# Kernel tuning notes

Hardware: AMD Instinct MI355X
Metric: run time of the kernel (lower is better)

## Reference

```python
import jax, jax.numpy as jnp
import numpy as np

B, S, HID = 2, 2048, 2048
NH, NKV, HD = 16, 16, 128
SCALE = 1.0 / np.sqrt(HD)


def _rotate_half(x):
    x1, x2 = jnp.split(x, 2, axis=-1)
    return jnp.concatenate([-x2, x1], axis=-1)


def setup_inputs() -> dict:
    key = jax.random.key(0)
    k1, k2, k3 = jax.random.split(key, 3)
    hidden_states = jax.random.normal(k1, (B, S, HID), dtype=jnp.float32)
    # standard RoPE cos/sin tables, shape [S, HD]
    inv_freq = 1.0 / (10000.0 ** (np.arange(0, HD, 2, dtype=np.float32) / HD))
    freqs = np.outer(np.arange(S, dtype=np.float32), inv_freq)  # [S, HD/2]
    emb = np.concatenate([freqs, freqs], axis=-1)               # [S, HD]
    cos = jnp.asarray(np.cos(emb), dtype=jnp.float32)
    sin = jnp.asarray(np.sin(emb), dtype=jnp.float32)
    # torch Linear weights are [out, in]; forward computes x @ W.T
    w_qkv = jax.random.normal(k2, ((NH + 2 * NKV) * HD, HID), dtype=jnp.float32) * 0.02
    w_o = jax.random.normal(k3, (HID, NH * HD), dtype=jnp.float32) * 0.02
    return {"hidden_states": hidden_states, "cos": cos, "sin": sin,
            "w_qkv": w_qkv, "w_o": w_o}


def reference(hidden_states, cos, sin, w_qkv, w_o):
    b, s, _ = hidden_states.shape
    qkv = hidden_states @ w_qkv.T                         # [B,S,(NH+2*NKV)*HD]
    qkv = qkv.reshape(b, s, NH + 2 * NKV, HD)
    q = qkv[:, :, :NH]                                    # [B,S,NH,HD]
    k = qkv[:, :, NH:NH + NKV]                            # [B,S,NKV,HD]
    v = qkv[:, :, NH + NKV:]                              # [B,S,NKV,HD]
    # RoPE: broadcast cos/sin [S,HD] -> [1,S,1,HD]
    c = cos[None, :, None, :]
    sn = sin[None, :, None, :]
    q = q * c + _rotate_half(q) * sn
    k = k * c + _rotate_half(k) * sn
    scores = jnp.einsum("bihd,bjhd->bhij", q, k) * SCALE  # [B,H,S,S]
    attn = jax.nn.softmax(scores, axis=-1)
    out = jnp.einsum("bhij,bjhd->bihd", attn, v)          # [B,S,H,HD]
    out = out.reshape(b, s, NH * HD)
    return out @ w_o.T                                    # [B,S,HID]
```

## Files before the change

kernel.cpp:

```cpp
#include <hip/hip_runtime.h>
#include <hip/hip_bf16.h>

typedef float f32x4 __attribute__((ext_vector_type(4)));
typedef __bf16 bf16x8 __attribute__((ext_vector_type(8)));
typedef __bf16 bf16x4 __attribute__((ext_vector_type(4)));

#define S_LEN 2048
#define NHEADS 16
#define HDIM 128
#define KLOG2E (0.08838834764831845f * 1.4426950408889634f)
#define MSHIFT 2.0f

__device__ __forceinline__ void gld_lds16(const __bf16* g, __bf16* l) {
  __builtin_amdgcn_global_load_lds(
      (__attribute__((address_space(1))) void*)(void*)g,
      (__attribute__((address_space(3))) void*)l,
      16, 0, 0);
}

template <int N>
__device__ __forceinline__ void waitv() {
  if constexpr (N == 8)      asm volatile("s_waitcnt vmcnt(8)" ::: "memory");
  else if constexpr (N == 6) asm volatile("s_waitcnt vmcnt(6)" ::: "memory");
  else if constexpr (N == 4) asm volatile("s_waitcnt vmcnt(4)" ::: "memory");
  else if constexpr (N == 3) asm volatile("s_waitcnt vmcnt(3)" ::: "memory");
  else                       asm volatile("s_waitcnt vmcnt(0)" ::: "memory");
}

__global__ __launch_bounds__(256)
void cvt_all(const float* __restrict__ i0, __bf16* __restrict__ o0,
             const float* __restrict__ i1, __bf16* __restrict__ o1,
             const float* __restrict__ i2, __bf16* __restrict__ o2) {
  int i = (blockIdx.x * 256 + threadIdx.x) * 4;
  if (i >= 25165824) return;
  const float* in;
  __bf16* out;
  if (i < 8388608)       { in = i0 + i;              out = o0 + i; }
  else if (i < 20971520) { in = i1 + (i - 8388608);  out = o1 + (i - 8388608); }
  else                   { in = i2 + (i - 20971520); out = o2 + (i - 20971520); }
  float4 v = *(const float4*)in;
  bf16x4 o;
  o[0] = (__bf16)v.x; o[1] = (__bf16)v.y; o[2] = (__bf16)v.z; o[3] = (__bf16)v.w;
  *(bf16x4*)out = o;
}

template <int MREP, bool RMAP>
__device__ __forceinline__ void gemm_core(const __bf16* __restrict__ A,
                                          const __bf16* __restrict__ B,
                                          __bf16* lds, int am0, int bn0,
                                          f32x4 (&acc)[MREP][4]) {
  constexpr int K = 2048;
  constexpr int AF = MREP * 2;
  constexpr int SLOT = (AF + 16) * 512;
  constexpr int NA = AF / 8;
  constexpr int NL = NA + 2;
  const int tid = threadIdx.x;
  const int w = tid >> 6, lane = tid & 63;
  const int l15 = lane & 15;
  const int wm = w >> 2, wn = w & 3;

  const __bf16* asrc = A + (size_t)(am0 + l15) * K + (lane >> 4) * 8;
  const __bf16* bsrc = B + (size_t)(bn0 + l15) * K + (lane >> 4) * 8;

  auto stage = [&](int t) {
    __bf16* s = lds + (t & 3) * SLOT;
#pragma unroll
    for (int i = 0; i < NA; ++i) {
      const int f = w * NA + i;
      gld_lds16(asrc + (size_t)f * (16 * K) + t * 32, s + f * 512 + lane * 8);
    }
#pragma unroll
    for (int i = 0; i < 2; ++i) {
      const int g = w * 2 + i;
      gld_lds16(bsrc + (size_t)g * (16 * K) + t * 32, s + (AF + g) * 512 + lane * 8);
    }
  };

  stage(0); stage(1); stage(2);
  waitv<2 * NL>();
  __builtin_amdgcn_s_barrier();

  for (int t = 0; t < 64; ++t) {
    if (t < 61) stage(t + 3);
    const __bf16* s = lds + (t & 3) * SLOT + lane * 8;
    const __bf16* sB = s + AF * 512;
    bf16x8 bfr[4];
#pragma unroll
    for (int j = 0; j < 4; ++j) {
      const int g = RMAP ? ((wn >> 1) * 8 + (wn & 1) * 2 + (j & 1) + (j >> 1) * 4)
                         : (wn * 4 + j);
      bfr[j] = *(const bf16x8*)(sB + g * 512);
    }
#pragma unroll
    for (int half = 0; half < MREP / 4; ++half) {
      bf16x8 af[4];
#pragma unroll
      for (int i = 0; i < 4; ++i)
        af[i] = *(const bf16x8*)(s + (wm * MREP + half * 4 + i) * 512);
      __builtin_amdgcn_s_setprio(1);
#pragma unroll
      for (int i = 0; i < 4; ++i)
#pragma unroll
        for (int j = 0; j < 4; ++j)
          acc[half * 4 + i][j] = __builtin_amdgcn_mfma_f32_16x16x32_bf16(
              af[i], bfr[j], acc[half * 4 + i][j], 0, 0, 0);
      __builtin_amdgcn_s_setprio(0);
    }
    if (t < 63) {
      if (t < 61)       waitv<2 * NL>();
      else if (t == 61) waitv<NL>();
      else              waitv<0>();
      __builtin_amdgcn_s_barrier();
    }
  }
}


__global__ __launch_bounds__(512)
void gemm_bt_qkp(const __bf16* __restrict__ A, const __bf16* __restrict__ B,
                 __bf16* __restrict__ Qp, __bf16* __restrict__ Kp,
                 const float* __restrict__ cosp, const float* __restrict__ sinp) {
  __shared__ alignas(16) char smem[139264];
  const int am0 = blockIdx.y * 256;
  const int bn0 = blockIdx.x * 256;
  const int tid = threadIdx.x;
  const int w = tid >> 6, lane = tid & 63;
  const int l15 = lane & 15, quad = lane >> 4;
  const int wm = w >> 2, wn = w & 3;
  f32x4 acc[8][4] = {};
  gemm_core<8, true>(A, B, (__bf16*)smem, am0, bn0, acc);

  __syncthreads();
  float* csb = (float*)smem;
  float* snb = csb + 256 * 68;
  const int sbase = am0 & 2047;
  for (int q = tid; q < 4096; q += 512) {
    const int row = q >> 4, dq = (q & 15) * 4;
    *(float4*)(csb + row * 68 + dq) =
        *(const float4*)(cosp + (size_t)(sbase + row) * 128 + dq);
    *(float4*)(snb + row * 68 + dq) =
        *(const float4*)(sinp + (size_t)(sbase + row) * 128 + dq);
  }
  __syncthreads();

  const int head_sel = wn >> 1;
  const int hcol0 = bn0 + head_sel * 128;
  const int head = hcol0 >> 7;
  const int h = head & 15;
  __bf16* dst = (head < 16) ? Qp : Kp;
#pragma unroll
  for (int i = 0; i < 8; ++i) {
    const int row_b = am0 + wm * 128 + i * 16 + quad * 4;
    const int bidx = row_b >> 11;
    const int s = row_b & 2047;
    const int sl = wm * 128 + i * 16 + quad * 4;
    const int s16 = s >> 4;
    const int l15p0 = s & 15;
#pragma unroll
    for (int j2 = 0; j2 < 2; ++j2) {
      const int dl = (wn & 1) * 32 + j2 * 16 + l15;
      const int dh = dl + 64;
      const int kkl = dl >> 5, qpl = (dl >> 3) & 3, el = dl & 7;
      const int kkh = dh >> 5, qph = (dh >> 3) & 3, eh = dh & 7;
      const size_t base_lo =
          (((size_t)((bidx * 16 + h) * 128 + s16) * 4 + kkl) * 64 + qpl * 16 + l15p0) * 8 + el;
      const size_t base_hi =
          (((size_t)((bidx * 16 + h) * 128 + s16) * 4 + kkh) * 64 + qph * 16 + l15p0) * 8 + eh;
#pragma unroll
      for (int r = 0; r < 4; ++r) {
        const float c = csb[(sl + r) * 68 + dl];
        const float sn = snb[(sl + r) * 68 + dl];
        const float a = acc[i][j2][r], bb = acc[i][j2 + 2][r];
        dst[base_lo + (size_t)r * 8] = (__bf16)(a * c - bb * sn);
        dst[base_hi + (size_t)r * 8] = (__bf16)(bb * c + a * sn);
      }
    }
  }
}

__global__ __launch_bounds__(512)
void gemm_bt_vp(const __bf16* __restrict__ A, const __bf16* __restrict__ B,
                __bf16* __restrict__ Vp) {
  __shared__ alignas(16) __bf16 lds[4 * 24 * 512];
  const int am0 = blockIdx.y * 128;
  const int bn0 = blockIdx.x * 256;
  const int tid = threadIdx.x;
  const int w = tid >> 6, lane = tid & 63;
  const int l15 = lane & 15, quad = lane >> 4;
  const int wm = w >> 2, wn = w & 3;
  f32x4 acc[4][4] = {};
  gemm_core<4, false>(A, B, lds, am0, bn0, acc);
#pragma unroll
  for (int i = 0; i < 4; ++i) {
    const int row_b = am0 + wm * 64 + i * 16 + quad * 4;
    const int b = row_b >> 11;
    const int key0 = row_b & 2047;
    const int quadp = (key0 >> 3) & 3;
    const int kkv = key0 >> 5;
    const int e0 = key0 & 7;
#pragma unroll
    for (int j = 0; j < 4; ++j) {
      const int col = bn0 + wn * 64 + j * 16 + l15;
      const int h = col >> 7, dd = col & 127;
      const int tt = dd >> 4, l15p = dd & 15;
      bf16x4 o;
#pragma unroll
      for (int r = 0; r < 4; ++r) o[r] = (__bf16)acc[i][j][r];
      size_t addr = (((size_t)((b * 16 + h) * 8 + tt) * 64 + kkv) * 64
                     + quadp * 16 + l15p) * 8 + e0;
      *(bf16x4*)(Vp + addr) = o;
    }
  }
}

__global__ __launch_bounds__(512)
void gemm_bt_f(const __bf16* __restrict__ A, const __bf16* __restrict__ B,
               float* __restrict__ C) {
  __shared__ alignas(16) __bf16 lds[4 * 24 * 512];
  const int am0 = blockIdx.y * 128;
  const int bn0 = blockIdx.x * 256;
  const int tid = threadIdx.x;
  const int w = tid >> 6, lane = tid & 63;
  const int l15 = lane & 15, quad = lane >> 4;
  const int wm = w >> 2, wn = w & 3;
  f32x4 acc[4][4] = {};
  gemm_core<4, false>(A, B, lds, am0, bn0, acc);
#pragma unroll
  for (int i = 0; i < 4; ++i) {
    const int row_b = am0 + wm * 64 + i * 16 + quad * 4;
#pragma unroll
    for (int j = 0; j < 4; ++j) {
      const int col = bn0 + wn * 64 + j * 16 + l15;
#pragma unroll
      for (int r = 0; r < 4; ++r)
        C[(size_t)(row_b + r) * 2048 + col] = acc[i][j][r];
    }
  }
}

__global__ __launch_bounds__(512)
void attn_kernel(const __bf16* __restrict__ Qp, const __bf16* __restrict__ Kp,
                 const __bf16* __restrict__ Vp, __bf16* __restrict__ O) {
  const int lid = blockIdx.x;
  const int qt = (lid >> 3) & 7;
  const int bh = (lid & 7) * 4 + (lid >> 6);
  const int b = bh >> 4, h = bh & 15;
  const int tid = threadIdx.x;
  const int w = tid >> 6;
  const int lane = tid & 63;
  const int l15 = lane & 15, quad = lane >> 4;

  __shared__ alignas(16) __bf16 KV[3][32 * 512];
  __shared__ alignas(16) __bf16 Ps[8][16][72];

  const __bf16* qbase = Qp + (size_t)bh * 262144 + lane * 8;
  const __bf16* kbase = Kp + (size_t)bh * 262144 + lane * 8;
  const __bf16* vbase = Vp + (size_t)bh * 262144 + lane * 8;

  bf16x8 qf[2][4];
#pragma unroll
  for (int qb = 0; qb < 2; ++qb)
#pragma unroll
    for (int kk = 0; kk < 4; ++kk)
      qf[qb][kk] =
          *(const bf16x8*)(qbase + (size_t)((qt * 16 + qb * 8 + w) * 4 + kk) * 512);

  bf16x8 onesf;
#pragma unroll
  for (int e = 0; e < 8; ++e) onesf[e] = (__bf16)1.0f;

  f32x4 o_acc[2][8] = {};
  f32x4 o_sum[2] = {};

  auto stage = [&](int tile) {
    __bf16* s = &KV[tile % 3][0];
#pragma unroll
    for (int ii = 0; ii < 2; ++ii) {
      const int c = w * 2 + ii;
      gld_lds16(kbase + ((size_t)tile * 16 + c) * 512, s + c * 512 + lane * 8);
      gld_lds16(vbase + (size_t)((c >> 1) * 64 + tile * 2 + (c & 1)) * 512,
                s + (16 + c) * 512 + lane * 8);
    }
  };

  stage(0);
  stage(1);
  waitv<4>();
  __builtin_amdgcn_s_barrier();

  for (int t = 0; t < 32; ++t) {
    if (t + 2 < 32) stage(t + 2);
    const __bf16* kvs = &KV[t % 3][0] + lane * 8;

    f32x4 sc[2][4] = {};
    __builtin_amdgcn_s_setprio(1);
#pragma unroll
    for (int kk = 0; kk < 4; ++kk) {
#pragma unroll
      for (int tt = 0; tt < 4; ++tt) {
        bf16x8 kf = *(const bf16x8*)(kvs + (tt * 4 + kk) * 512);
        sc[0][tt] = __builtin_amdgcn_mfma_f32_16x16x32_bf16(qf[0][kk], kf, sc[0][tt], 0, 0, 0);
        sc[1][tt] = __builtin_amdgcn_mfma_f32_16x16x32_bf16(qf[1][kk], kf, sc[1][tt], 0, 0, 0);
      }
    }
    __builtin_amdgcn_s_setprio(0);

    bf16x8 a[2][2];
#pragma unroll
    for (int qb = 0; qb < 2; ++qb) {
#pragma unroll
      for (int tt = 0; tt < 4; ++tt)
#pragma unroll
        for (int r = 0; r < 4; ++r)
          Ps[w][quad * 4 + r][tt * 16 + l15] =
              (__bf16)exp2f(sc[qb][tt][r] * KLOG2E - MSHIFT);
      a[qb][0] = *(const bf16x8*)&Ps[w][l15][quad * 8];
      a[qb][1] = *(const bf16x8*)&Ps[w][l15][32 + quad * 8];
    }

    __builtin_amdgcn_s_setprio(1);
#pragma unroll
    for (int kk = 0; kk < 2; ++kk) {
      o_sum[0] = __builtin_amdgcn_mfma_f32_16x16x32_bf16(a[0][kk], onesf, o_sum[0], 0, 0, 0);
      o_sum[1] = __builtin_amdgcn_mfma_f32_16x16x32_bf16(a[1][kk], onesf, o_sum[1], 0, 0, 0);
#pragma unroll
      for (int tt = 0; tt < 8; ++tt) {
        bf16x8 vf = *(const bf16x8*)(kvs + (16 + tt * 2 + kk) * 512);
        o_acc[0][tt] = __builtin_amdgcn_mfma_f32_16x16x32_bf16(a[0][kk], vf, o_acc[0][tt], 0, 0, 0);
        o_acc[1][tt] = __builtin_amdgcn_mfma_f32_16x16x32_bf16(a[1][kk], vf, o_acc[1][tt], 0, 0, 0);
      }
    }
    __builtin_amdgcn_s_setprio(0);

    if (t < 31) {
      asm volatile("s_waitcnt lgkmcnt(0)" ::: "memory");
      if (t < 30) waitv<4>();
      else        waitv<0>();
      __builtin_amdgcn_s_barrier();
    }
  }

#pragma unroll
  for (int qb = 0; qb < 2; ++qb) {
    float inv[4];
#pragma unroll
    for (int r = 0; r < 4; ++r) inv[r] = 1.0f / o_sum[qb][r];
    const int row0 = qt * 256 + (qb * 8 + w) * 16 + quad * 4;
#pragma unroll
    for (int tt = 0; tt < 8; ++tt)
#pragma unroll
      for (int r = 0; r < 4; ++r)
        O[(size_t)(b * S_LEN + row0 + r) * 2048 + h * HDIM + tt * 16 + l15] =
            (__bf16)(o_acc[qb][tt][r] * inv[r]);
  }
}

extern "C" void kernel_launch(void* const* d_in, const int* in_sizes, int n_in,
                              void* d_out, int out_size, void* d_ws, size_t ws_size,
                              hipStream_t stream) {
  const float* hs   = (const float*)d_in[0];
  const float* cosp = (const float*)d_in[1];
  const float* sinp = (const float*)d_in[2];
  const float* wqkv = (const float*)d_in[3];
  const float* wo   = (const float*)d_in[4];
  float* out = (float*)d_out;

  char* ws = (char*)d_ws;
  __bf16* Xb   = (__bf16*)(ws);
  __bf16* Obuf = (__bf16*)(ws);
  __bf16* Wqb  = (__bf16*)(ws + 16777216);
  __bf16* Wob  = (__bf16*)(ws + 41943040);
  __bf16* Qp   = (__bf16*)(ws + 50331648);
  __bf16* Kp   = (__bf16*)(ws + 67108864);
  __bf16* Vp   = (__bf16*)(ws + 83886080);
  if (ws_size < 100663296) return;

  cvt_all<<<24576, 256, 0, stream>>>(hs, Xb, wqkv, Wqb, wo, Wob);

  gemm_bt_qkp<<<dim3(16, 16), 512, 0, stream>>>(Xb, Wqb, Qp, Kp, cosp, sinp);
  gemm_bt_vp<<<dim3(8, 32), 512, 0, stream>>>(Xb, Wqb + 8388608, Vp);
  attn_kernel<<<256, 512, 0, stream>>>(Qp, Kp, Vp, Obuf);
  gemm_bt_f<<<dim3(8, 32), 512, 0, stream>>>(Obuf, Wob, out);
}
```

Before: 408.1 us.

## Halve attention block size, double-buffer K/V separately, swizzle P layout

The attention kernel now runs 512 blocks of 256 threads, each covering 128 queries, instead of 256 blocks of 512 threads. The three-deep mixed K/V ring becomes separate double-buffered K and V LDS tiles. The next tile's copy is issued mid-iteration, after a barrier that follows the score phase. The QK MFMA operands are swapped, so each lane writes contiguous 4-element P vectors into an XOR-swizzled per-wave LDS buffer, which is meant to cut bank conflicts and scalar stores. The smaller blocks aim to fill more CUs and raise occupancy, at the cost of less prefetch depth and an extra barrier per iteration.

```diff
diff --git a/kernel.cpp b/kernel.cpp
--- a/kernel.cpp
+++ b/kernel.cpp
@@ -238,20 +238,21 @@
   }
 }
 
-__global__ __launch_bounds__(512)
+__global__ __launch_bounds__(256, 4)
 void attn_kernel(const __bf16* __restrict__ Qp, const __bf16* __restrict__ Kp,
                  const __bf16* __restrict__ Vp, __bf16* __restrict__ O) {
   const int lid = blockIdx.x;
-  const int qt = (lid >> 3) & 7;
-  const int bh = (lid & 7) * 4 + (lid >> 6);
+  const int qt = (lid >> 3) & 15;
+  const int bh = (lid & 7) * 4 + (lid >> 7);
   const int b = bh >> 4, h = bh & 15;
   const int tid = threadIdx.x;
   const int w = tid >> 6;
   const int lane = tid & 63;
   const int l15 = lane & 15, quad = lane >> 4;
 
-  __shared__ alignas(16) __bf16 KV[3][32 * 512];
-  __shared__ alignas(16) __bf16 Ps[8][16][72];
+  __shared__ alignas(16) __bf16 Kls[2][16 * 512];
+  __shared__ alignas(16) __bf16 Vls[2][16 * 512];
+  __shared__ alignas(16) __bf16 Ps[4][16 * 64];
 
   const __bf16* qbase = Qp + (size_t)bh * 262144 + lane * 8;
   const __bf16* kbase = Kp + (size_t)bh * 262144 + lane * 8;
@@ -263,7 +264,7 @@
 #pragma unroll
     for (int kk = 0; kk < 4; ++kk)
       qf[qb][kk] =
-          *(const bf16x8*)(qbase + (size_t)((qt * 16 + qb * 8 + w) * 4 + kk) * 512);
+          *(const bf16x8*)(qbase + (size_t)((qt * 8 + qb * 4 + w) * 4 + kk) * 512);
 
   bf16x8 onesf;
 #pragma unroll
@@ -272,25 +273,32 @@
   f32x4 o_acc[2][8] = {};
   f32x4 o_sum[2] = {};
 
+  const int swz = (l15 & 7) << 3;
+  __bf16* psw = &Ps[w][l15 * 64];
+
   auto stage = [&](int tile) {
-    __bf16* s = &KV[tile % 3][0];
-#pragma unroll
-    for (int ii = 0; ii < 2; ++ii) {
-      const int c = w * 2 + ii;
-      gld_lds16(kbase + ((size_t)tile * 16 + c) * 512, s + c * 512 + lane * 8);
+    __bf16* ks = &Kls[tile & 1][0];
+    __bf16* vs = &Vls[tile & 1][0];
+#pragma unroll
+    for (int ii = 0; ii < 4; ++ii) {
+      const int c = w * 4 + ii;
+      gld_lds16(kbase + ((size_t)tile * 16 + c) * 512, ks + c * 512 + lane * 8);
+    }
+#pragma unroll
+    for (int ii = 0; ii < 4; ++ii) {
+      const int c = w * 4 + ii;
       gld_lds16(vbase + (size_t)((c >> 1) * 64 + tile * 2 + (c & 1)) * 512,
-                s + (16 + c) * 512 + lane * 8);
+                vs + c * 512 + lane * 8);
     }
   };
 
   stage(0);
-  stage(1);
   waitv<4>();
   __builtin_amdgcn_s_barrier();
 
   for (int t = 0; t < 32; ++t) {
-    if (t + 2 < 32) stage(t + 2);
-    const __bf16* kvs = &KV[t % 3][0] + lane * 8;
+    const __bf16* ks = &Kls[t & 1][0] + lane * 8;
+    const __bf16* vs = &Vls[t & 1][0] + lane * 8;
 
     f32x4 sc[2][4] = {};
     __builtin_amdgcn_s_setprio(1);
@@ -298,44 +306,48 @@
     for (int kk = 0; kk < 4; ++kk) {
 #pragma unroll
       for (int tt = 0; tt < 4; ++tt) {
-        bf16x8 kf = *(const bf16x8*)(kvs + (tt * 4 + kk) * 512);
-        sc[0][tt] = __builtin_amdgcn_mfma_f32_16x16x32_bf16(qf[0][kk], kf, sc[0][tt], 0, 0, 0);
-        sc[1][tt] = __builtin_amdgcn_mfma_f32_16x16x32_bf16(qf[1][kk], kf, sc[1][tt], 0, 0, 0);
+        bf16x8 kf = *(const bf16x8*)(ks + (tt * 4 + kk) * 512);
+        sc[0][tt] = __builtin_amdgcn_mfma_f32_16x16x32_bf16(kf, qf[0][kk], sc[0][tt], 0, 0, 0);
+        sc[1][tt] = __builtin_amdgcn_mfma_f32_16x16x32_bf16(kf, qf[1][kk], sc[1][tt], 0, 0, 0);
       }
     }
     __builtin_amdgcn_s_setprio(0);
 
-    bf16x8 a[2][2];
+    bf16x8 pa[2][2];
 #pragma unroll
     for (int qb = 0; qb < 2; ++qb) {
 #pragma unroll
-      for (int tt = 0; tt < 4; ++tt)
+      for (int tt = 0; tt < 4; ++tt) {
+        bf16x4 o;
 #pragma unroll
         for (int r = 0; r < 4; ++r)
-          Ps[w][quad * 4 + r][tt * 16 + l15] =
-              (__bf16)exp2f(sc[qb][tt][r] * KLOG2E - MSHIFT);
-      a[qb][0] = *(const bf16x8*)&Ps[w][l15][quad * 8];
-      a[qb][1] = *(const bf16x8*)&Ps[w][l15][32 + quad * 8];
-    }
+          o[r] = (__bf16)exp2f(sc[qb][tt][r] * KLOG2E - MSHIFT);
+        *(bf16x4*)(psw + ((tt * 16 + quad * 4) ^ swz)) = o;
+      }
+      pa[qb][0] = *(const bf16x8*)(psw + ((quad * 8) ^ swz));
+      pa[qb][1] = *(const bf16x8*)(psw + ((32 + quad * 8) ^ swz));
+    }
+
+    waitv<0>();
+    __builtin_amdgcn_s_barrier();
+    if (t < 31) stage(t + 1);
 
     __builtin_amdgcn_s_setprio(1);
 #pragma unroll
     for (int kk = 0; kk < 2; ++kk) {
-      o_sum[0] = __builtin_amdgcn_mfma_f32_16x16x32_bf16(a[0][kk], onesf, o_sum[0], 0, 0, 0);
-      o_sum[1] = __builtin_amdgcn_mfma_f32_16x16x32_bf16(a[1][kk], onesf, o_sum[1], 0, 0, 0);
+      o_sum[0] = __builtin_amdgcn_mfma_f32_16x16x32_bf16(pa[0][kk], onesf, o_sum[0], 0, 0, 0);
+      o_sum[1] = __builtin_amdgcn_mfma_f32_16x16x32_bf16(pa[1][kk], onesf, o_sum[1], 0, 0, 0);
 #pragma unroll
       for (int tt = 0; tt < 8; ++tt) {
-        bf16x8 vf = *(const bf16x8*)(kvs + (16 + tt * 2 + kk) * 512);
-        o_acc[0][tt] = __builtin_amdgcn_mfma_f32_16x16x32_bf16(a[0][kk], vf, o_acc[0][tt], 0, 0, 0);
-        o_acc[1][tt] = __builtin_amdgcn_mfma_f32_16x16x32_bf16(a[1][kk], vf, o_acc[1][tt], 0, 0, 0);
+        bf16x8 vf = *(const bf16x8*)(vs + (tt * 2 + kk) * 512);
+        o_acc[0][tt] = __builtin_amdgcn_mfma_f32_16x16x32_bf16(pa[0][kk], vf, o_acc[0][tt], 0, 0, 0);
+        o_acc[1][tt] = __builtin_amdgcn_mfma_f32_16x16x32_bf16(pa[1][kk], vf, o_acc[1][tt], 0, 0, 0);
       }
     }
     __builtin_amdgcn_s_setprio(0);
 
     if (t < 31) {
-      asm volatile("s_waitcnt lgkmcnt(0)" ::: "memory");
-      if (t < 30) waitv<4>();
-      else        waitv<0>();
+      waitv<4>();
       __builtin_amdgcn_s_barrier();
     }
   }
@@ -345,7 +357,7 @@
     float inv[4];
 #pragma unroll
     for (int r = 0; r < 4; ++r) inv[r] = 1.0f / o_sum[qb][r];
-    const int row0 = qt * 256 + (qb * 8 + w) * 16 + quad * 4;
+    const int row0 = qt * 128 + (qb * 4 + w) * 16 + quad * 4;
 #pragma unroll
     for (int tt = 0; tt < 8; ++tt)
 #pragma unroll
@@ -379,6 +391,6 @@
 
   gemm_bt_qkp<<<dim3(16, 16), 512, 0, stream>>>(Xb, Wqb, Qp, Kp, cosp, sinp);
   gemm_bt_vp<<<dim3(8, 32), 512, 0, stream>>>(Xb, Wqb + 8388608, Vp);
-  attn_kernel<<<256, 512, 0, stream>>>(Qp, Kp, Vp, Obuf);
+  attn_kernel<<<512, 256, 0, stream>>>(Qp, Kp, Vp, Obuf);
   gemm_bt_f<<<dim3(8, 32), 512, 0, stream>>>(Obuf, Wob, out);
 }
```

Result: no change. 401.8 us (-1.5%).
